# Optimization experiments

Measured on AMD Instinct MI355X. Metric: run time of the kernel, lower is better.

## Reference

```python
import jax, jax.numpy as jnp
import numpy as np

D_MODEL = 768
HEADS = 4
HEAD_DIM = D_MODEL // HEADS
SCALE = 20.0  # source divides scores by hard-coded 20
NEG = -1e9
LN_EPS = 1e-5


def setup_inputs() -> dict:
    key = jax.random.key(0)
    ks = jax.random.split(key, 8)
    B, S = 4, 2048
    x = jax.random.normal(ks[0], (B, S, D_MODEL), dtype=jnp.float32)
    attention_mask = jnp.zeros((B, 1, S), dtype=bool)  # no padding
    s = 1.0 / np.sqrt(D_MODEL)
    Wq = jax.random.normal(ks[1], (D_MODEL, D_MODEL), dtype=jnp.float32) * s
    Wk = jax.random.normal(ks[2], (D_MODEL, D_MODEL), dtype=jnp.float32) * s
    Wv = jax.random.normal(ks[3], (D_MODEL, D_MODEL), dtype=jnp.float32) * s
    bq = jnp.zeros((D_MODEL,), jnp.float32)
    bk = jnp.zeros((D_MODEL,), jnp.float32)
    bv = jnp.zeros((D_MODEL,), jnp.float32)
    gamma = jnp.ones((D_MODEL,), jnp.float32)
    beta = jnp.zeros((D_MODEL,), jnp.float32)
    return {"x": x, "attention_mask": attention_mask, "Wq": Wq, "bq": bq,
            "Wk": Wk, "bk": bk, "Wv": Wv, "bv": bv, "gamma": gamma, "beta": beta}


def _split_heads(t, B, S):
    return t.reshape(B, S, HEADS, HEAD_DIM).transpose(0, 2, 1, 3)  # [B,H,S,D]


def reference(x, attention_mask, Wq, bq, Wk, bk, Wv, bv, gamma, beta):
    B, S, _ = x.shape
    Q = _split_heads(x @ Wq.T + bq, B, S)
    K = _split_heads(x @ Wk.T + bk, B, S)
    V = _split_heads(x @ Wv.T + bv, B, S)
    # scores [B,H,Sq,Sk]
    w = jnp.einsum('bhqd,bhkd->bhqk', Q, K) / SCALE
    pad = attention_mask[:, :, :, None]                     # [B,1,S,1] -> broadcast
    look = jnp.triu(jnp.ones((S, S), dtype=bool), 1)        # strict upper triangle
    mask = look[None, None] | pad
    w = jnp.where(mask, NEG, w)
    # NOTE: source uses Softmax(dim=2), i.e. over the QUERY axis — kept faithfully
    attn = jax.nn.softmax(w, axis=2)
    x1 = jnp.einsum('bhqk,bhkd->bhqd', attn, V)             # [B,H,S,D]
    x1 = x1.transpose(0, 2, 1, 3).reshape(B, S, D_MODEL)
    y = x + x1
    mu = jnp.mean(y, axis=-1, keepdims=True)
    var = jnp.mean((y - mu) ** 2, axis=-1, keepdims=True)
    return (y - mu) * jax.lax.rsqrt(var + LN_EPS) * gamma + beta
```

## Files before the change

### kernel.cpp

```cpp
#include <hip/hip_runtime.h>

typedef _Float16 f16;
typedef _Float16 f16x8 __attribute__((ext_vector_type(8)));
typedef _Float16 f16x4 __attribute__((ext_vector_type(4)));
typedef float    f32x4 __attribute__((ext_vector_type(4)));

#define MFMA16(a,b,c) __builtin_amdgcn_mfma_f32_16x16x32_f16(a,b,c,0,0,0)

static constexpr float NEGV = -1e9f;
static constexpr float SC   = 0.05f;


__device__ __forceinline__ void gload16(const void* g, void* l){
    __builtin_amdgcn_global_load_lds(
        (const __attribute__((address_space(1))) void*)g,
        (__attribute__((address_space(3))) void*)l, 16, 0, 0);
}

__global__ __launch_bounds__(256) void cvt_kernel(const float* __restrict__ in,
                                                  f16* __restrict__ out, int n){
    int i = (blockIdx.x*256 + threadIdx.x)*4;
    if (i < n){
        float4 v = *reinterpret_cast<const float4*>(in + i);
        f16x4 o = { (f16)v.x, (f16)v.y, (f16)v.z, (f16)v.w };
        *reinterpret_cast<f16x4*>(out + i) = o;
    }
}

__global__ __launch_bounds__(256) void zero_kernel(float* __restrict__ p, int n){
    int i = (blockIdx.x*256 + threadIdx.x)*4;
    if (i < n){
        float4 z = {0.f,0.f,0.f,0.f};
        *reinterpret_cast<float4*>(p + i) = z;
    }
}

__global__ __launch_bounds__(256) void proj_kernel(
    const f16* __restrict__ xb, const f16* __restrict__ Wb,
    const float* __restrict__ bq, const float* __restrict__ bk, const float* __restrict__ bv,
    f16* __restrict__ Qb, f16* __restrict__ Kb, f16* __restrict__ Vt)
{
    __shared__ f16 As[128*32];
    __shared__ f16 Bs[128*32];
    const int z = blockIdx.z;
    const f16*   Wz   = Wb + (size_t)z*768*768;
    const float* bias = (z==0) ? bq : (z==1 ? bk : bv);
    f16*         out  = (z==0) ? Qb : (z==1 ? Kb : Vt);
    const int row0 = blockIdx.y*128, n0 = blockIdx.x*128;
    const int tid = threadIdx.x, w = tid>>6, l = tid&63;
    const int wm = w>>1, wn = w&1, c = l&15, g = l>>4;
    f32x4 zero = {0.f,0.f,0.f,0.f};
    f32x4 acc[4][4];
    for (int i=0;i<4;i++) for (int j=0;j<4;j++) acc[i][j] = zero;

    const f16* ag = xb + (size_t)(row0 + w*32 + (l>>2))*768 + (l&3)*8;
    const f16* bg = Wz + (size_t)(n0   + w*32 + (l>>2))*768 + (l&3)*8;
    f16* asd = As + w*1024;
    f16* bsd = Bs + w*1024;

    for (int k0 = 0; k0 < 768; k0 += 32){
        __syncthreads();
        gload16(ag + k0,          asd      );
        gload16(ag + k0 + 16*768, asd + 512);
        gload16(bg + k0,          bsd      );
        gload16(bg + k0 + 16*768, bsd + 512);
        __syncthreads();
        f16x8 af[4], bf[4];
        for (int mt=0; mt<4; mt++)
            af[mt] = *reinterpret_cast<const f16x8*>(As + (wm*64 + mt*16 + c)*32 + g*8);
        for (int nt=0; nt<4; nt++)
            bf[nt] = *reinterpret_cast<const f16x8*>(Bs + (wn*64 + nt*16 + c)*32 + g*8);
        for (int mt=0; mt<4; mt++)
            for (int nt=0; nt<4; nt++)
                acc[mt][nt] = MFMA16(af[mt], bf[nt], acc[mt][nt]);
    }

    for (int nt=0; nt<4; nt++){
        int nb = n0 + wn*64 + nt*16;
        int h  = nb/192;
        int d  = (nb - h*192) + c;
        float bv_ = bias[nb + c];
        for (int mt=0; mt<4; mt++){
            int mb = row0 + wm*64 + mt*16 + g*4;
            int bi = mb>>11, s0 = mb&2047;
            int bh = bi*4 + h;
            if (z < 2){
                int ds = d>>5, gg = (d>>3)&3, e = d&7;
                for (int r=0;r<4;r++){
                    int s = s0 + r;
                    out[ ((size_t)(bh*128 + (s>>4))*6 + ds)*512 + ((gg*16) + (s&15))*8 + e ]
                        = (f16)(acc[mt][nt][r] + bv_);
                }
            } else {
                int dt = d>>4, cV = d&15;
                int kb64 = s0>>6, ks = (s0>>5)&1, gk = (s0>>3)&3, e0 = s0&7;
                f16x4 pk = { (f16)(acc[mt][nt][0] + bv_), (f16)(acc[mt][nt][1] + bv_),
                             (f16)(acc[mt][nt][2] + bv_), (f16)(acc[mt][nt][3] + bv_) };
                *reinterpret_cast<f16x4*>(
                    &out[ ((size_t)(bh*32 + kb64)*24 + dt*2 + ks)*512 + (gk*16 + cV)*8 + e0 ]) = pk;
            }
        }
    }
}

__global__ __launch_bounds__(512,4) void colstats_kernel(
    const f16* __restrict__ Qb, const f16* __restrict__ Kb,
    const unsigned char* __restrict__ am,
    float* __restrict__ Mp, float* __restrict__ Lp)
{
    __shared__ f16 Qs[2][24*512];
    const int bh = blockIdx.z, b = bh>>2;
    const int ch = blockIdx.y;
    const int kb = blockIdx.x;
    const int tid = threadIdx.x, w = tid>>6, l = tid&63;
    const int c = l&15, g = l>>4;
    const int kt = kb*128 + w*16;
    const f16* Qfm = Qb + (size_t)bh*128*6*512;
    const unsigned char* amb = am + b*2048;

    f16x8 kf[6];
    {
        const f16* kbase = Kb + ((size_t)(bh*128 + kb*8 + w)*6)*512 + l*8;
        for (int ds=0; ds<6; ds++) kf[ds] = *reinterpret_cast<const f16x8*>(kbase + ds*512);
    }

    float M = -1e38f, L = 0.f;
    f32x4 zero = {0.f,0.f,0.f,0.f};
    const int qt0 = max(ch*512, kb*128);
    const int qt1 = ch*512 + 512;
    const int nt  = (qt1 - qt0) >> 6;

    if (nt > 0){
        const int cid = w*3;
        {
            const f16* src = Qfm + ((size_t)(qt0>>4)*6 + cid)*512 + l*8;
            gload16(src,        &Qs[0][cid*512]);
            gload16(src + 512,  &Qs[0][(cid+1)*512]);
            gload16(src + 1024, &Qs[0][(cid+2)*512]);
        }
        __syncthreads();
        for (int it=0; it<nt; it++){
            int cur = it&1;
            if (it+1 < nt){
                const f16* src = Qfm + ((size_t)((qt0 + (it+1)*64)>>4)*6 + cid)*512 + l*8;
                gload16(src,        &Qs[cur^1][cid*512]);
                gload16(src + 512,  &Qs[cur^1][(cid+1)*512]);
                gload16(src + 1024, &Qs[cur^1][(cid+2)*512]);
            }
            int qt = qt0 + it*64;
            for (int j2=0; j2<4; j2++){
                int q0 = qt + j2*16;
                if (q0 + 15 < kt) continue;
                f32x4 sacc = zero;
                for (int ds=0; ds<6; ds++){
                    f16x8 qfr = *reinterpret_cast<const f16x8*>(&Qs[cur][(j2*6+ds)*512 + l*8]);
                    sacc = MFMA16(qfr, kf[ds], sacc);
                }
                float sv[4]; float m4 = -1e38f;
                for (int r=0;r<4;r++){
                    int q = q0 + g*4 + r;
                    float v = sacc[r]*SC;
                    if (amb[q]) v = NEGV;
                    if (q < kt + c) v = -1e38f;
                    sv[r] = v; m4 = fmaxf(m4, v);
                }
                m4 = fmaxf(m4, __shfl_xor(m4, 16));
                m4 = fmaxf(m4, __shfl_xor(m4, 32));
                float Mn = fmaxf(M, m4);
                float p = __expf(sv[0]-Mn) + __expf(sv[1]-Mn) + __expf(sv[2]-Mn) + __expf(sv[3]-Mn);
                p += __shfl_xor(p, 16);
                p += __shfl_xor(p, 32);
                L = L*__expf(M - Mn) + p;
                M = Mn;
            }
            __syncthreads();
        }
    }
    if (l < 16){
        size_t o = ((size_t)bh*4 + ch)*2048 + kt + l;
        Mp[o] = M;
        Lp[o] = L;
    }
}

__global__ __launch_bounds__(256) void combine_kernel(
    const float* __restrict__ Mp, const float* __restrict__ Lp,
    float* __restrict__ Mst, float* __restrict__ Lst)
{
    int idx = blockIdx.x*256 + threadIdx.x;
    int bh = idx >> 11, col = idx & 2047;
    float m[4];
    float M = -1e38f;
    for (int ch=0; ch<4; ch++){
        m[ch] = Mp[((size_t)bh*4 + ch)*2048 + col];
        M = fmaxf(M, m[ch]);
    }
    float L = 0.f;
    for (int ch=0; ch<4; ch++)
        L += Lp[((size_t)bh*4 + ch)*2048 + col] * __expf(m[ch] - M);
    Mst[(size_t)bh*2048 + col] = M;
    Lst[(size_t)bh*2048 + col] = 1.f/L;
}

__global__ __launch_bounds__(512,4) void attn_kernel(
    const f16* __restrict__ Qb, const f16* __restrict__ Kb, const f16* __restrict__ Vt,
    const float* __restrict__ Mst, const float* __restrict__ Lst,
    const unsigned char* __restrict__ am,
    float* __restrict__ x1)
{
    __shared__ f16 Ks[2][12*512];
    __shared__ f16 Vs[2][12*512];
    __shared__ f16 Pl[8][16*32];
    const int bh = blockIdx.z, b = bh>>2, h = bh&3;
    const int qb = blockIdx.x;
    const int ch = blockIdx.y;
    if (qb < 4*ch) return;
    const int tid = threadIdx.x, w = tid>>6, l = tid&63;
    const int c = l&15, g = l>>4;
    const int qw = qb*128 + w*16;
    const f16* Kfm = Kb + (size_t)bh*128*6*512;
    const f16* Vfm = Vt + (size_t)bh*32*24*512;
    const float* Mh = Mst + (size_t)bh*2048;
    const float* Lh = Lst + (size_t)bh*2048;
    char* Pb = (char*)(&Pl[w][0]);

    f16x8 qf[6];
    {
        const f16* qbase = Qb + ((size_t)(bh*128 + (qw>>4))*6)*512 + l*8;
        for (int ds=0; ds<6; ds++) qf[ds] = *reinterpret_cast<const f16x8*>(qbase + ds*512);
    }
    bool pm[4];
    for (int r=0;r<4;r++) pm[r] = am[b*2048 + qw + g*4 + r] != 0;

    f32x4 zero = {0.f,0.f,0.f,0.f};
    f32x4 acc[12];
    for (int i=0;i<12;i++) acc[i] = zero;

    const int k00  = ch*512;
    const int kend = min(ch*512 + 512, qb*128 + 128);
    const int nt   = (kend - k00) >> 5;

    const int cid = w*3;

    auto stage = [&](int buf, int k0){
        for (int i=0;i<3;i++){
            int ci = cid + i;
            if (ci < 12){
                int tl = ci/6, ds = ci - tl*6;
                gload16(Kfm + ((size_t)((k0>>4) + tl)*6 + ds)*512 + l*8, &Ks[buf][ci*512]);
            } else {
                int dt = ci - 12;
                int ks = (k0>>5)&1;
                gload16(Vfm + ((size_t)(k0>>6)*24 + dt*2 + ks)*512 + l*8, &Vs[buf][dt*512]);
            }
        }
    };

    stage(0, k00);
    __syncthreads();
    for (int it=0; it<nt; it++){
        int cur = it&1;
        int k0  = k00 + it*32;
        if (it+1 < nt) stage(cur^1, k0 + 32);

        if (k0 <= qw + 15){
            for (int kt2=0; kt2<2; kt2++){
                int kk = k0 + kt2*16;
                f32x4 sacc = zero;
                for (int ds=0; ds<6; ds++){
                    f16x8 kfr = *reinterpret_cast<const f16x8*>(&Ks[cur][(kt2*6+ds)*512 + l*8]);
                    sacc = MFMA16(qf[ds], kfr, sacc);
                }
                float Mk = Mh[kk + c], iL = Lh[kk + c];
                for (int r=0;r<4;r++){
                    int q = qw + g*4 + r;
                    float v = sacc[r]*SC;
                    if (pm[r]) v = NEGV;
                    float p = __expf(v - Mk)*iL;
                    if (kk + c > q) p = 0.f;
                    int row = g*4 + r;
                    int byo = (row*64 + (kt2*16 + c)*2) ^ ((row&3)<<4);
                    *reinterpret_cast<f16*>(Pb + byo) = (f16)p;
                }
            }
            {
                int byo = (c*64 + g*16) ^ ((c&3)<<4);
                f16x8 pa = *reinterpret_cast<const f16x8*>(Pb + byo);
                for (int dt=0; dt<12; dt++){
                    f16x8 vb = *reinterpret_cast<const f16x8*>(&Vs[cur][dt*512 + l*8]);
                    acc[dt] = MFMA16(pa, vb, acc[dt]);
                }
            }
        }
        __syncthreads();
    }
    for (int dt=0; dt<12; dt++){
        int d = h*192 + dt*16 + c;
        for (int r=0;r<4;r++){
            int q = qw + g*4 + r;
            atomicAdd(&x1[(size_t)(b*2048 + q)*768 + d], acc[dt][r]);
        }
    }
}

__global__ __launch_bounds__(256) void ln_kernel(
    const float* __restrict__ x, const float* __restrict__ x1,
    const float* __restrict__ gamma, const float* __restrict__ beta,
    float* __restrict__ out)
{
    const int r = blockIdx.x, t = threadIdx.x;
    const float* xr = x  + (size_t)r*768;
    const float* yr = x1 + (size_t)r*768;
    float v[3]; float s1 = 0.f, s2 = 0.f;
    for (int i=0;i<3;i++){ int j = t + i*256; float y = xr[j] + yr[j]; v[i]=y; s1+=y; s2+=y*y; }
    for (int o=32;o>=1;o>>=1){ s1 += __shfl_xor(s1,o); s2 += __shfl_xor(s2,o); }
    __shared__ float a1[4], a2[4];
    if ((t&63)==0){ a1[t>>6]=s1; a2[t>>6]=s2; }
    __syncthreads();
    s1 = a1[0]+a1[1]+a1[2]+a1[3];
    s2 = a2[0]+a2[1]+a2[2]+a2[3];
    float mu  = s1*(1.f/768.f);
    float var = s2*(1.f/768.f) - mu*mu;
    float rs  = rsqrtf(var + 1e-5f);
    for (int i=0;i<3;i++){
        int j = t + i*256;
        out[(size_t)r*768 + j] = (v[i]-mu)*rs*gamma[j] + beta[j];
    }
}

extern "C" void kernel_launch(void* const* d_in, const int* in_sizes, int n_in,
                              void* d_out, int out_size, void* d_ws, size_t ws_size,
                              hipStream_t stream)
{
    const float* x     = (const float*)d_in[0];
    const unsigned char* am = (const unsigned char*)d_in[1];
    const float* Wq    = (const float*)d_in[2];
    const float* bq    = (const float*)d_in[3];
    const float* Wk    = (const float*)d_in[4];
    const float* bk    = (const float*)d_in[5];
    const float* Wv    = (const float*)d_in[6];
    const float* bv    = (const float*)d_in[7];
    const float* gamma = (const float*)d_in[8];
    const float* beta  = (const float*)d_in[9];
    float* out = (float*)d_out;

    f16* xb  = (f16*)d_ws;
    f16* Wb  = xb + (size_t)8192*768;
    f16* Qb  = Wb + (size_t)3*768*768;
    f16* Kb  = Qb + (size_t)16*2048*192;
    f16* Vt  = Kb + (size_t)16*2048*192;
    float* Mst = (float*)(Vt + (size_t)16*2048*192);
    float* Lst = Mst + 16*2048;
    float* x1  = Lst + 16*2048;
    float* Mp  = (float*)xb;
    float* Lp  = Mp + 16*4*2048;

    cvt_kernel<<<6144, 256, 0, stream>>>(x,  xb, 8192*768);
    cvt_kernel<<<576,  256, 0, stream>>>(Wq, Wb,            589824);
    cvt_kernel<<<576,  256, 0, stream>>>(Wk, Wb + 589824,   589824);
    cvt_kernel<<<576,  256, 0, stream>>>(Wv, Wb + 2*589824, 589824);
    proj_kernel<<<dim3(6,64,3), 256, 0, stream>>>(xb, Wb, bq, bk, bv, Qb, Kb, Vt);
    colstats_kernel<<<dim3(16,4,16), 512, 0, stream>>>(Qb, Kb, am, Mp, Lp);
    combine_kernel<<<128, 256, 0, stream>>>(Mp, Lp, Mst, Lst);
    zero_kernel<<<6144, 256, 0, stream>>>(x1, 8192*768);
    attn_kernel<<<dim3(16,4,16), 512, 0, stream>>>(Qb, Kb, Vt, Mst, Lst, am, x1);
    ln_kernel<<<8192, 256, 0, stream>>>(x, x1, gamma, beta, out);
}
```

Measured before the change: 304.1 us.

## Materialize exponentiated scores once and fold column normalization into V

Replaces the two-pass colstats plus attention flow, which computes QK^T twice, with a single pass. That pass writes exp(scores) as f16 to a packed lower-triangular buffer and accumulates query-axis column sums with atomics. V is then divided by those column sums, and a separate PV kernel multiplies the stored probabilities by the scaled V, writing x1 directly with no zeroing or atomic accumulation. The cost is a large global write and read of the probability tile (about 68 MB), and the max-subtraction stabilization is dropped. The new path runs only when the workspace is big enough, otherwise the old path is kept.

```diff
diff --git a/kernel.cpp b/kernel.cpp
--- a/kernel.cpp
+++ b/kernel.cpp
@@ -10,6 +10,11 @@
 static constexpr float NEGV = -1e9f;
 static constexpr float SC   = 0.05f;
 
+
+__device__ __forceinline__ int poff(int qt){
+    int m = qt>>1;
+    return qt + m*(m-1) + ((qt&1) ? m : 0);
+}
 
 __device__ __forceinline__ void gload16(const void* g, void* l){
     __builtin_amdgcn_global_load_lds(
@@ -103,6 +108,171 @@
     }
 }
 
+__global__ __launch_bounds__(512,4) void qkexp_kernel(
+    const f16* __restrict__ Qb, const f16* __restrict__ Kb,
+    const unsigned char* __restrict__ am,
+    float* __restrict__ L, f16* __restrict__ Pg)
+{
+    __shared__ f16 Ks[2][12*512];
+    __shared__ f16 Pl[8][16*32];
+    const int bh = blockIdx.z, b = bh>>2;
+    const int qb = blockIdx.x;
+    const int ch = blockIdx.y;
+    if (qb < 4*ch) return;
+    const int tid = threadIdx.x, w = tid>>6, l = tid&63;
+    const int c = l&15, g = l>>4;
+    const int qt = qb*8 + w, qw = qt*16;
+    const f16* Kfm = Kb + (size_t)bh*128*6*512;
+    char* Pb = (char*)(&Pl[w][0]);
+    f16* pw = Pg + ((size_t)bh*4160 + poff(qt))*512 + l*8;
+    float* Lb = L + bh*2048;
+
+    f16x8 qf[6];
+    {
+        const f16* qbase = Qb + ((size_t)(bh*128 + qt)*6)*512 + l*8;
+        for (int ds=0; ds<6; ds++) qf[ds] = *reinterpret_cast<const f16x8*>(qbase + ds*512);
+    }
+    bool pm[4];
+    for (int r=0;r<4;r++) pm[r] = am[b*2048 + qw + g*4 + r] != 0;
+
+    f32x4 zero = {0.f,0.f,0.f,0.f};
+    const int k00  = ch*512;
+    const int kend = min(ch*512 + 512, qb*128 + 128);
+    const int nt   = (kend - k00) >> 5;
+    const int cid  = w*3;
+
+    auto stage = [&](int buf, int k0){
+        for (int i=0;i<3;i++){
+            int ci = cid + i;
+            if (ci < 12){
+                int tl = ci/6, ds = ci - tl*6;
+                gload16(Kfm + ((size_t)((k0>>4) + tl)*6 + ds)*512 + l*8, &Ks[buf][ci*512]);
+            }
+        }
+    };
+
+    stage(0, k00);
+    __syncthreads();
+    for (int it=0; it<nt; it++){
+        int cur = it&1;
+        int k0  = k00 + it*32;
+        if (it+1 < nt) stage(cur^1, k0 + 32);
+
+        if (k0 <= qw + 15){
+            float cs[2];
+            for (int kt2=0; kt2<2; kt2++){
+                int kk = k0 + kt2*16;
+                f32x4 sacc = zero;
+                for (int ds=0; ds<6; ds++){
+                    f16x8 kfr = *reinterpret_cast<const f16x8*>(&Ks[cur][(kt2*6+ds)*512 + l*8]);
+                    sacc = MFMA16(qf[ds], kfr, sacc);
+                }
+                float csl = 0.f;
+                for (int r=0;r<4;r++){
+                    int q = qw + g*4 + r;
+                    float v = sacc[r]*SC;
+                    if (pm[r]) v = NEGV;
+                    float p = __expf(v);
+                    if (kk + c > q) p = 0.f;
+                    csl += p;
+                    int row = g*4 + r;
+                    int byo = (row*64 + (kt2*16 + c)*2) ^ ((row&3)<<4);
+                    *reinterpret_cast<f16*>(Pb + byo) = (f16)p;
+                }
+                csl += __shfl_xor(csl, 16);
+                csl += __shfl_xor(csl, 32);
+                cs[kt2] = csl;
+            }
+            {
+                int byo = (c*64 + g*16) ^ ((c&3)<<4);
+                f16x8 pa = *reinterpret_cast<const f16x8*>(Pb + byo);
+                *reinterpret_cast<f16x8*>(pw + (size_t)(k0>>5)*512) = pa;
+            }
+            if (l < 32){
+                float csv = (l < 16) ? cs[0] : cs[1];
+                int kcol = k0 + ((l < 16) ? 0 : 16) + (l & 15);
+                atomicAdd(&Lb[kcol], csv);
+            }
+        }
+        __syncthreads();
+    }
+}
+
+__global__ __launch_bounds__(256) void scalev_kernel(f16* __restrict__ V, const float* __restrict__ L){
+    int idx = blockIdx.x*256 + threadIdx.x;
+    size_t base = (size_t)idx * 8;
+    int bh = idx / 49152;
+    int rem = idx - bh*49152;
+    int chunk = rem >> 6;
+    int sl = rem & 63;
+    int kb64 = chunk/24, cr = chunk - kb64*24;
+    int ks = cr & 1;
+    int gk = sl >> 4;
+    int k0 = kb64*64 + ks*32 + gk*8;
+    const float* Lb = L + bh*2048 + k0;
+    f16x8 v = *reinterpret_cast<f16x8*>(V + base);
+    f16x8 o;
+    for (int e=0;e<8;e++){
+        float Lv = fmaxf(Lb[e], 1e-30f);
+        o[e] = (f16)((float)v[e] / Lv);
+    }
+    *reinterpret_cast<f16x8*>(V + base) = o;
+}
+
+__global__ __launch_bounds__(512,4) void pv_kernel(
+    const f16* __restrict__ Pg, const f16* __restrict__ Vt,
+    float* __restrict__ x1)
+{
+    __shared__ f16 Vs[2][12*512];
+    const int bh = blockIdx.z, b = bh>>2, h = bh&3;
+    const int qb = 15 - blockIdx.x;
+    const int tid = threadIdx.x, w = tid>>6, l = tid&63;
+    const int c = l&15, g = l>>4;
+    const int qt = qb*8 + w, qw = qt*16;
+    const f16* Vfm = Vt + (size_t)bh*32*24*512;
+    const f16* pp  = Pg + ((size_t)bh*4160 + poff(qt))*512 + l*8;
+
+    f32x4 zero = {0.f,0.f,0.f,0.f};
+    f32x4 acc[12];
+    for (int i=0;i<12;i++) acc[i] = zero;
+
+    const int nt  = 4*qb + 4;
+    const int cid = w*3;
+
+    auto stage = [&](int buf, int k0){
+        for (int i=0;i<3;i++){
+            int ci = cid + i;
+            if (ci < 12){
+                gload16(Vfm + ((size_t)(k0>>6)*24 + ci*2 + ((k0>>5)&1))*512 + l*8, &Vs[buf][ci*512]);
+            }
+        }
+    };
+
+    stage(0, 0);
+    __syncthreads();
+    for (int it=0; it<nt; it++){
+        int cur = it&1;
+        int k0  = it*32;
+        if (it+1 < nt) stage(cur^1, k0 + 32);
+
+        if (k0 <= qw + 15){
+            f16x8 pa = *reinterpret_cast<const f16x8*>(pp + (size_t)(k0>>5)*512);
+            for (int dt=0; dt<12; dt++){
+                f16x8 vb = *reinterpret_cast<const f16x8*>(&Vs[cur][dt*512 + l*8]);
+                acc[dt] = MFMA16(pa, vb, acc[dt]);
+            }
+        }
+        __syncthreads();
+    }
+    for (int dt=0; dt<12; dt++){
+        int d = h*192 + dt*16 + c;
+        for (int r=0;r<4;r++){
+            int q = qw + g*4 + r;
+            x1[(size_t)(b*2048 + q)*768 + d] = acc[dt][r];
+        }
+    }
+}
+
 __global__ __launch_bounds__(512,4) void colstats_kernel(
     const f16* __restrict__ Qb, const f16* __restrict__ Kb,
     const unsigned char* __restrict__ am,
@@ -239,7 +409,6 @@
     const int k00  = ch*512;
     const int kend = min(ch*512 + 512, qb*128 + 128);
     const int nt   = (kend - k00) >> 5;
-
     const int cid = w*3;
 
     auto stage = [&](int buf, int k0){
@@ -349,20 +518,33 @@
     f16* Qb  = Wb + (size_t)3*768*768;
     f16* Kb  = Qb + (size_t)16*2048*192;
     f16* Vt  = Kb + (size_t)16*2048*192;
-    float* Mst = (float*)(Vt + (size_t)16*2048*192);
-    float* Lst = Mst + 16*2048;
-    float* x1  = Lst + 16*2048;
-    float* Mp  = (float*)xb;
-    float* Lp  = Mp + 16*4*2048;
+    f16* Pg  = Vt + (size_t)16*2048*192;
+    const size_t NEED_NEW = 12582912ULL + 3538944 + 3*12582912 + 68157440;
 
     cvt_kernel<<<6144, 256, 0, stream>>>(x,  xb, 8192*768);
     cvt_kernel<<<576,  256, 0, stream>>>(Wq, Wb,            589824);
     cvt_kernel<<<576,  256, 0, stream>>>(Wk, Wb + 589824,   589824);
     cvt_kernel<<<576,  256, 0, stream>>>(Wv, Wb + 2*589824, 589824);
     proj_kernel<<<dim3(6,64,3), 256, 0, stream>>>(xb, Wb, bq, bk, bv, Qb, Kb, Vt);
-    colstats_kernel<<<dim3(16,4,16), 512, 0, stream>>>(Qb, Kb, am, Mp, Lp);
-    combine_kernel<<<128, 256, 0, stream>>>(Mp, Lp, Mst, Lst);
-    zero_kernel<<<6144, 256, 0, stream>>>(x1, 8192*768);
-    attn_kernel<<<dim3(16,4,16), 512, 0, stream>>>(Qb, Kb, Vt, Mst, Lst, am, x1);
-    ln_kernel<<<8192, 256, 0, stream>>>(x, x1, gamma, beta, out);
-}
+
+    if (ws_size >= NEED_NEW){
+        float* L  = (float*)xb;
+        float* x1 = (float*)Qb;
+        zero_kernel<<<32, 256, 0, stream>>>(L, 16*2048);
+        qkexp_kernel<<<dim3(16,4,16), 512, 0, stream>>>(Qb, Kb, am, L, Pg);
+        scalev_kernel<<<3072, 256, 0, stream>>>(Vt, L);
+        pv_kernel<<<dim3(16,1,16), 512, 0, stream>>>(Pg, Vt, x1);
+        ln_kernel<<<8192, 256, 0, stream>>>(x, x1, gamma, beta, out);
+    } else {
+        float* Mst = (float*)(Vt + (size_t)16*2048*192);
+        float* Lst = Mst + 16*2048;
+        float* x1  = Lst + 16*2048;
+        float* Mp  = (float*)xb;
+        float* Lp  = Mp + 16*4*2048;
+        colstats_kernel<<<dim3(16,4,16), 512, 0, stream>>>(Qb, Kb, am, Mp, Lp);
+        combine_kernel<<<128, 256, 0, stream>>>(Mp, Lp, Mst, Lst);
+        zero_kernel<<<6144, 256, 0, stream>>>(x1, 8192*768);
+        attn_kernel<<<dim3(16,4,16), 512, 0, stream>>>(Qb, Kb, Vt, Mst, Lst, am, x1);
+        ln_kernel<<<8192, 256, 0, stream>>>(x, x1, gamma, beta, out);
+    }
+}
```

Result: faster. 288.9 us (-5.0%).

## Compute QK once, store exp scores, fold column normalization into V

Applied to the files above, without the earlier changes.

Replaces the column-stat pass plus recompute attention with one kernel that computes QK^T once, stores unnormalized exp scores to a global buffer, and accumulates per-key column sums atomically. A small kernel scales V by the inverse column sums, and a PV kernel reads the stored probabilities. The aim is to remove the duplicate QK matmul and the stats combine step. In exchange it adds a large global write and read of the probability matrix and many atomics. Dropping max subtraction also relies on scores staying small. It additionally merges the three weight conversions into one launch.

```diff
diff --git a/kernel.cpp b/kernel.cpp
--- a/kernel.cpp
+++ b/kernel.cpp
@@ -10,6 +10,11 @@
 static constexpr float NEGV = -1e9f;
 static constexpr float SC   = 0.05f;
 
+
+__device__ __forceinline__ int poff(int qt){
+    int m = qt>>1;
+    return qt + m*(m-1) + ((qt&1) ? m : 0);
+}
 
 __device__ __forceinline__ void gload16(const void* g, void* l){
     __builtin_amdgcn_global_load_lds(
@@ -25,6 +30,20 @@
         f16x4 o = { (f16)v.x, (f16)v.y, (f16)v.z, (f16)v.w };
         *reinterpret_cast<f16x4*>(out + i) = o;
     }
+}
+
+__global__ __launch_bounds__(256) void cvtw_kernel(const float* __restrict__ a,
+                                                   const float* __restrict__ b,
+                                                   const float* __restrict__ c,
+                                                   f16* __restrict__ out){
+    int idx = blockIdx.x*256 + threadIdx.x;
+    int which = idx / 147456;
+    int r = idx - which*147456;
+    const float* src = (which==0) ? a : (which==1 ? b : c);
+    int i = r*4;
+    float4 v = *reinterpret_cast<const float4*>(src + i);
+    f16x4 o = { (f16)v.x, (f16)v.y, (f16)v.z, (f16)v.w };
+    *reinterpret_cast<f16x4*>(out + (size_t)which*589824 + i) = o;
 }
 
 __global__ __launch_bounds__(256) void zero_kernel(float* __restrict__ p, int n){
@@ -103,134 +122,133 @@
     }
 }
 
-__global__ __launch_bounds__(512,4) void colstats_kernel(
+__global__ __launch_bounds__(512,4) void qkexp_kernel(
     const f16* __restrict__ Qb, const f16* __restrict__ Kb,
     const unsigned char* __restrict__ am,
-    float* __restrict__ Mp, float* __restrict__ Lp)
-{
-    __shared__ f16 Qs[2][24*512];
+    float* __restrict__ L, f16* __restrict__ Pg)
+{
+    __shared__ f16 Ks[2][24*512];
+    __shared__ f16 Pl[8][16*32];
     const int bh = blockIdx.z, b = bh>>2;
+    const int qb = blockIdx.x;
     const int ch = blockIdx.y;
-    const int kb = blockIdx.x;
+    if (qb < 4*ch) return;
     const int tid = threadIdx.x, w = tid>>6, l = tid&63;
     const int c = l&15, g = l>>4;
-    const int kt = kb*128 + w*16;
-    const f16* Qfm = Qb + (size_t)bh*128*6*512;
-    const unsigned char* amb = am + b*2048;
-
-    f16x8 kf[6];
+    const int qt = qb*8 + w, qw = qt*16;
+    const f16* Kfm = Kb + (size_t)bh*128*6*512;
+    char* Pb = (char*)(&Pl[w][0]);
+    f16* pw = Pg + ((size_t)bh*4160 + poff(qt))*512 + l*8;
+    float* Lb = L + bh*2048;
+
+    f16x8 qf[6];
     {
-        const f16* kbase = Kb + ((size_t)(bh*128 + kb*8 + w)*6)*512 + l*8;
-        for (int ds=0; ds<6; ds++) kf[ds] = *reinterpret_cast<const f16x8*>(kbase + ds*512);
-    }
-
-    float M = -1e38f, L = 0.f;
+        const f16* qbase = Qb + ((size_t)(bh*128 + qt)*6)*512 + l*8;
+        for (int ds=0; ds<6; ds++) qf[ds] = *reinterpret_cast<const f16x8*>(qbase + ds*512);
+    }
+    bool pm[4];
+    for (int r=0;r<4;r++) pm[r] = am[b*2048 + qw + g*4 + r] != 0;
+
     f32x4 zero = {0.f,0.f,0.f,0.f};
-    const int qt0 = max(ch*512, kb*128);
-    const int qt1 = ch*512 + 512;
-    const int nt  = (qt1 - qt0) >> 6;
-
-    if (nt > 0){
-        const int cid = w*3;
-        {
-            const f16* src = Qfm + ((size_t)(qt0>>4)*6 + cid)*512 + l*8;
-            gload16(src,        &Qs[0][cid*512]);
-            gload16(src + 512,  &Qs[0][(cid+1)*512]);
-            gload16(src + 1024, &Qs[0][(cid+2)*512]);
+    const int k00  = ch*512;
+    const int kend = min(ch*512 + 512, qb*128 + 128);
+    const int nt   = (kend - k00) >> 6;
+    const int cid  = w*3;
+
+    auto stage = [&](int buf, int k0){
+        for (int i=0;i<3;i++){
+            int ci = cid + i;
+            int tl = ci/6, ds = ci - tl*6;
+            gload16(Kfm + ((size_t)((k0>>4) + tl)*6 + ds)*512 + l*8, &Ks[buf][ci*512]);
+        }
+    };
+
+    stage(0, k00);
+    __syncthreads();
+    for (int it=0; it<nt; it++){
+        int cur = it&1;
+        int k0  = k00 + it*64;
+        if (it+1 < nt) stage(cur^1, k0 + 64);
+
+        for (int half=0; half<2; half++){
+            int kh = k0 + half*32;
+            if (kh <= qw + 15){
+                float cs[2];
+                for (int kt2=0; kt2<2; kt2++){
+                    int ktile = half*2 + kt2;
+                    int kk = k0 + ktile*16;
+                    f32x4 sacc = zero;
+                    for (int ds=0; ds<6; ds++){
+                        f16x8 kfr = *reinterpret_cast<const f16x8*>(&Ks[cur][(ktile*6+ds)*512 + l*8]);
+                        sacc = MFMA16(qf[ds], kfr, sacc);
+                    }
+                    float csl = 0.f;
+                    for (int r=0;r<4;r++){
+                        int q = qw + g*4 + r;
+                        float v = sacc[r]*SC;
+                        if (pm[r]) v = NEGV;
+                        float p = __expf(v);
+                        if (kk + c > q) p = 0.f;
+                        csl += p;
+                        int row = g*4 + r;
+                        int byo = (row*64 + (kt2*16 + c)*2) ^ ((row&3)<<4);
+                        *reinterpret_cast<f16*>(Pb + byo) = (f16)p;
+                    }
+                    csl += __shfl_xor(csl, 16);
+                    csl += __shfl_xor(csl, 32);
+                    cs[kt2] = csl;
+                }
+                {
+                    int byo = (c*64 + g*16) ^ ((c&3)<<4);
+                    f16x8 pa = *reinterpret_cast<const f16x8*>(Pb + byo);
+                    *reinterpret_cast<f16x8*>(pw + (size_t)(kh>>5)*512) = pa;
+                }
+                if (l < 32){
+                    float csv = (l < 16) ? cs[0] : cs[1];
+                    int kcol = kh + ((l < 16) ? 0 : 16) + (l & 15);
+                    atomicAdd(&Lb[kcol], csv);
+                }
+            }
         }
         __syncthreads();
-        for (int it=0; it<nt; it++){
-            int cur = it&1;
-            if (it+1 < nt){
-                const f16* src = Qfm + ((size_t)((qt0 + (it+1)*64)>>4)*6 + cid)*512 + l*8;
-                gload16(src,        &Qs[cur^1][cid*512]);
-                gload16(src + 512,  &Qs[cur^1][(cid+1)*512]);
-                gload16(src + 1024, &Qs[cur^1][(cid+2)*512]);
-            }
-            int qt = qt0 + it*64;
-            for (int j2=0; j2<4; j2++){
-                int q0 = qt + j2*16;
-                if (q0 + 15 < kt) continue;
-                f32x4 sacc = zero;
-                for (int ds=0; ds<6; ds++){
-                    f16x8 qfr = *reinterpret_cast<const f16x8*>(&Qs[cur][(j2*6+ds)*512 + l*8]);
-                    sacc = MFMA16(qfr, kf[ds], sacc);
-                }
-                float sv[4]; float m4 = -1e38f;
-                for (int r=0;r<4;r++){
-                    int q = q0 + g*4 + r;
-                    float v = sacc[r]*SC;
-                    if (amb[q]) v = NEGV;
-                    if (q < kt + c) v = -1e38f;
-                    sv[r] = v; m4 = fmaxf(m4, v);
-                }
-                m4 = fmaxf(m4, __shfl_xor(m4, 16));
-                m4 = fmaxf(m4, __shfl_xor(m4, 32));
-                float Mn = fmaxf(M, m4);
-                float p = __expf(sv[0]-Mn) + __expf(sv[1]-Mn) + __expf(sv[2]-Mn) + __expf(sv[3]-Mn);
-                p += __shfl_xor(p, 16);
-                p += __shfl_xor(p, 32);
-                L = L*__expf(M - Mn) + p;
-                M = Mn;
-            }
-            __syncthreads();
-        }
-    }
-    if (l < 16){
-        size_t o = ((size_t)bh*4 + ch)*2048 + kt + l;
-        Mp[o] = M;
-        Lp[o] = L;
-    }
-}
-
-__global__ __launch_bounds__(256) void combine_kernel(
-    const float* __restrict__ Mp, const float* __restrict__ Lp,
-    float* __restrict__ Mst, float* __restrict__ Lst)
-{
+    }
+}
+
+__global__ __launch_bounds__(256) void scalev_kernel(f16* __restrict__ V, const float* __restrict__ L){
     int idx = blockIdx.x*256 + threadIdx.x;
-    int bh = idx >> 11, col = idx & 2047;
-    float m[4];
-    float M = -1e38f;
-    for (int ch=0; ch<4; ch++){
-        m[ch] = Mp[((size_t)bh*4 + ch)*2048 + col];
-        M = fmaxf(M, m[ch]);
-    }
-    float L = 0.f;
-    for (int ch=0; ch<4; ch++)
-        L += Lp[((size_t)bh*4 + ch)*2048 + col] * __expf(m[ch] - M);
-    Mst[(size_t)bh*2048 + col] = M;
-    Lst[(size_t)bh*2048 + col] = 1.f/L;
-}
-
-__global__ __launch_bounds__(512,4) void attn_kernel(
-    const f16* __restrict__ Qb, const f16* __restrict__ Kb, const f16* __restrict__ Vt,
-    const float* __restrict__ Mst, const float* __restrict__ Lst,
-    const unsigned char* __restrict__ am,
+    size_t base = (size_t)idx * 8;
+    int bh = idx / 49152;
+    int rem = idx - bh*49152;
+    int chunk = rem >> 6;
+    int sl = rem & 63;
+    int kb64 = chunk/24, cr = chunk - kb64*24;
+    int ks = cr & 1;
+    int gk = sl >> 4;
+    int k0 = kb64*64 + ks*32 + gk*8;
+    const float* Lb = L + bh*2048 + k0;
+    f16x8 v = *reinterpret_cast<f16x8*>(V + base);
+    f16x8 o;
+    for (int e=0;e<8;e++){
+        float Lv = fmaxf(Lb[e], 1e-30f);
+        o[e] = (f16)((float)v[e] / Lv);
+    }
+    *reinterpret_cast<f16x8*>(V + base) = o;
+}
+
+__global__ __launch_bounds__(512,4) void pv_kernel(
+    const f16* __restrict__ Pg, const f16* __restrict__ Vt,
     float* __restrict__ x1)
 {
-    __shared__ f16 Ks[2][12*512];
     __shared__ f16 Vs[2][12*512];
-    __shared__ f16 Pl[8][16*32];
     const int bh = blockIdx.z, b = bh>>2, h = bh&3;
     const int qb = blockIdx.x;
     const int ch = blockIdx.y;
     if (qb < 4*ch) return;
     const int tid = threadIdx.x, w = tid>>6, l = tid&63;
     const int c = l&15, g = l>>4;
-    const int qw = qb*128 + w*16;
-    const f16* Kfm = Kb + (size_t)bh*128*6*512;
+    const int qt = qb*8 + w, qw = qt*16;
     const f16* Vfm = Vt + (size_t)bh*32*24*512;
-    const float* Mh = Mst + (size_t)bh*2048;
-    const float* Lh = Lst + (size_t)bh*2048;
-    char* Pb = (char*)(&Pl[w][0]);
-
-    f16x8 qf[6];
-    {
-        const f16* qbase = Qb + ((size_t)(bh*128 + (qw>>4))*6)*512 + l*8;
-        for (int ds=0; ds<6; ds++) qf[ds] = *reinterpret_cast<const f16x8*>(qbase + ds*512);
-    }
-    bool pm[4];
-    for (int r=0;r<4;r++) pm[r] = am[b*2048 + qw + g*4 + r] != 0;
+    const f16* pp  = Pg + ((size_t)bh*4160 + poff(qt))*512 + l*8;
 
     f32x4 zero = {0.f,0.f,0.f,0.f};
     f32x4 acc[12];
@@ -239,60 +257,36 @@
     const int k00  = ch*512;
     const int kend = min(ch*512 + 512, qb*128 + 128);
     const int nt   = (kend - k00) >> 5;
-
-    const int cid = w*3;
+    const int cid  = w*3;
 
     auto stage = [&](int buf, int k0){
         for (int i=0;i<3;i++){
             int ci = cid + i;
-            if (ci < 12){
-                int tl = ci/6, ds = ci - tl*6;
-                gload16(Kfm + ((size_t)((k0>>4) + tl)*6 + ds)*512 + l*8, &Ks[buf][ci*512]);
-            } else {
-                int dt = ci - 12;
-                int ks = (k0>>5)&1;
-                gload16(Vfm + ((size_t)(k0>>6)*24 + dt*2 + ks)*512 + l*8, &Vs[buf][dt*512]);
-            }
+            if (ci < 12)
+                gload16(Vfm + ((size_t)(k0>>6)*24 + ci*2 + ((k0>>5)&1))*512 + l*8, &Vs[buf][ci*512]);
         }
     };
 
     stage(0, k00);
+    f16x8 pa_cur = *reinterpret_cast<const f16x8*>(pp + (size_t)(k00>>5)*512);
     __syncthreads();
     for (int it=0; it<nt; it++){
         int cur = it&1;
         int k0  = k00 + it*32;
         if (it+1 < nt) stage(cur^1, k0 + 32);
 
+        f16x8 pa_next = pa_cur;
+        bool actn = (it+1 < nt) && (k0 + 32 <= qw + 15);
+        if (actn) pa_next = *reinterpret_cast<const f16x8*>(pp + (size_t)((k0+32)>>5)*512);
+
         if (k0 <= qw + 15){
-            for (int kt2=0; kt2<2; kt2++){
-                int kk = k0 + kt2*16;
-                f32x4 sacc = zero;
-                for (int ds=0; ds<6; ds++){
-                    f16x8 kfr = *reinterpret_cast<const f16x8*>(&Ks[cur][(kt2*6+ds)*512 + l*8]);
-                    sacc = MFMA16(qf[ds], kfr, sacc);
-                }
-                float Mk = Mh[kk + c], iL = Lh[kk + c];
-                for (int r=0;r<4;r++){
-                    int q = qw + g*4 + r;
-                    float v = sacc[r]*SC;
-                    if (pm[r]) v = NEGV;
-                    float p = __expf(v - Mk)*iL;
-                    if (kk + c > q) p = 0.f;
-                    int row = g*4 + r;
-                    int byo = (row*64 + (kt2*16 + c)*2) ^ ((row&3)<<4);
-                    *reinterpret_cast<f16*>(Pb + byo) = (f16)p;
-                }
+            for (int dt=0; dt<12; dt++){
+                f16x8 vb = *reinterpret_cast<const f16x8*>(&Vs[cur][dt*512 + l*8]);
+                acc[dt] = MFMA16(pa_cur, vb, acc[dt]);
             }
-            {
-                int byo = (c*64 + g*16) ^ ((c&3)<<4);
-                f16x8 pa = *reinterpret_cast<const f16x8*>(Pb + byo);
-                for (int dt=0; dt<12; dt++){
-                    f16x8 vb = *reinterpret_cast<const f16x8*>(&Vs[cur][dt*512 + l*8]);
-                    acc[dt] = MFMA16(pa, vb, acc[dt]);
-                }
-            }
         }
         __syncthreads();
+        pa_cur = pa_next;
     }
     for (int dt=0; dt<12; dt++){
         int d = h*192 + dt*16 + c;
@@ -349,20 +343,17 @@
     f16* Qb  = Wb + (size_t)3*768*768;
     f16* Kb  = Qb + (size_t)16*2048*192;
     f16* Vt  = Kb + (size_t)16*2048*192;
-    float* Mst = (float*)(Vt + (size_t)16*2048*192);
-    float* Lst = Mst + 16*2048;
-    float* x1  = Lst + 16*2048;
-    float* Mp  = (float*)xb;
-    float* Lp  = Mp + 16*4*2048;
+    f16* Pg  = Vt + (size_t)16*2048*192;
+    float* L  = (float*)xb;
+    float* x1 = (float*)Qb;
 
     cvt_kernel<<<6144, 256, 0, stream>>>(x,  xb, 8192*768);
-    cvt_kernel<<<576,  256, 0, stream>>>(Wq, Wb,            589824);
-    cvt_kernel<<<576,  256, 0, stream>>>(Wk, Wb + 589824,   589824);
-    cvt_kernel<<<576,  256, 0, stream>>>(Wv, Wb + 2*589824, 589824);
+    cvtw_kernel<<<1728, 256, 0, stream>>>(Wq, Wk, Wv, Wb);
     proj_kernel<<<dim3(6,64,3), 256, 0, stream>>>(xb, Wb, bq, bk, bv, Qb, Kb, Vt);
-    colstats_kernel<<<dim3(16,4,16), 512, 0, stream>>>(Qb, Kb, am, Mp, Lp);
-    combine_kernel<<<128, 256, 0, stream>>>(Mp, Lp, Mst, Lst);
+    zero_kernel<<<32, 256, 0, stream>>>(L, 16*2048);
+    qkexp_kernel<<<dim3(16,4,16), 512, 0, stream>>>(Qb, Kb, am, L, Pg);
     zero_kernel<<<6144, 256, 0, stream>>>(x1, 8192*768);
-    attn_kernel<<<dim3(16,4,16), 512, 0, stream>>>(Qb, Kb, Vt, Mst, Lst, am, x1);
+    scalev_kernel<<<3072, 256, 0, stream>>>(Vt, L);
+    pv_kernel<<<dim3(16,4,16), 512, 0, stream>>>(Pg, Vt, x1);
     ln_kernel<<<8192, 256, 0, stream>>>(x, x1, gamma, beta, out);
 }
```

Measured after the change: 301.2 us. About the same (-1.0%).
